# Kernel tuning notes

Hardware: AMD Instinct MI355X
Metric: run time of the kernel (lower is better)

The kernel has to match this reference:

```python
import jax, jax.numpy as jnp
import numpy as np

EPS = 1e-8  # matches torch.nn.functional.cosine_similarity default eps

def setup_inputs() -> dict:
    key = jax.random.key(0)
    k1, k2 = jax.random.split(key)
    x1 = jax.random.normal(k1, (8192, 1024), dtype=jnp.float32)
    x2 = jax.random.normal(k2, (8192, 1024), dtype=jnp.float32)
    return {"x1": x1, "x2": x2}

def reference(x1, x2):
    # cosine_similarity(x1[:,None,:], x2[None,:,:], dim=-1)
    # = (x1 . x2) / (max(||x1||,eps) * max(||x2||,eps))
    # Expressed as normalize-once + GEMM (same math, no [N,M,D] intermediate).
    n1 = jnp.maximum(jnp.linalg.norm(x1, axis=-1, keepdims=True), EPS)  # [N,1]
    n2 = jnp.maximum(jnp.linalg.norm(x2, axis=-1, keepdims=True), EPS)  # [M,1]
    x1n = x1 / n1
    x2n = x2 / n2
    return jnp.einsum('nd,md->nm', x1n, x2n)  # [N,M]
```

## Files before the change

kernel.cpp:

```cpp
#include <hip/hip_runtime.h>
#include <hip/hip_bf16.h>
#include <math.h>


typedef __bf16 bf16x8 __attribute__((ext_vector_type(8)));
typedef float  f32x4  __attribute__((ext_vector_type(4)));

#define LDSP(x) ((__attribute__((address_space(3))) void*)(x))
#define GLBP(x) ((const __attribute__((address_space(1))) void*)(x))

#define BM 256
#define BN 256
#define BK 64
#define EPS_CS 1e-8f


__global__ __launch_bounds__(256) void nrm_bf16_1024_2(const float* __restrict__ in1,
                                                       const float* __restrict__ in2,
                                                       __bf16* __restrict__ out1,
                                                       __bf16* __restrict__ out2,
                                                       int NR) {
    const int r = blockIdx.x;
    const float* in = (r < NR) ? in1 : in2;
    __bf16* out = (r < NR) ? out1 : out2;
    const int row = (r < NR) ? r : r - NR;
    const int t = threadIdx.x;
    const float4 v = reinterpret_cast<const float4*>(in + (size_t)row * 1024)[t];
    float ss = v.x * v.x + v.y * v.y + v.z * v.z + v.w * v.w;
#pragma unroll
    for (int off = 32; off > 0; off >>= 1) ss += __shfl_down(ss, off, 64);
    __shared__ float red[4];
    const int lane = t & 63, wid = t >> 6;
    if (lane == 0) red[wid] = ss;
    __syncthreads();
    const float tot = red[0] + red[1] + red[2] + red[3];
    const float rn = 1.0f / fmaxf(sqrtf(tot), EPS_CS);
    ushort4 pk;
    pk.x = __builtin_bit_cast(unsigned short, (__bf16)(v.x * rn));
    pk.y = __builtin_bit_cast(unsigned short, (__bf16)(v.y * rn));
    pk.z = __builtin_bit_cast(unsigned short, (__bf16)(v.z * rn));
    pk.w = __builtin_bit_cast(unsigned short, (__bf16)(v.w * rn));
    reinterpret_cast<ushort4*>(out + (size_t)row * 1024)[t] = pk;
}


__global__ __launch_bounds__(512, 2) void gemm_nt_bf16_256(const __bf16* __restrict__ A,
                                                           const __bf16* __restrict__ B,
                                                           float* __restrict__ C,
                                                           int NC, int D) {
    __shared__ alignas(16) __bf16 As[2][BM * BK];
    __shared__ alignas(16) __bf16 Bs[2][BN * BK];

    const int t    = threadIdx.x;
    const int lane = t & 63;
    const int wid  = t >> 6;
    const int wm   = wid >> 2;
    const int wn   = wid & 3;
    const int fr   = lane & 15;
    const int fq   = lane >> 4;
    const int xk   = fr & 7;
    const int g0   = fq ^ xk;
    const int g1   = (4 + fq) ^ xk;

    const int nwg = gridDim.x;
    int swz = blockIdx.x;
    if ((nwg & 7) == 0) swz = (swz & 7) * (nwg >> 3) + (swz >> 3);
    const int ntn  = NC / BN;
    const int brow = (swz / ntn) * BM;
    const int bcol = (swz % ntn) * BN;

    const int srow = t >> 3;
    const int sg8  = ((t & 7) ^ (srow & 7)) << 3;
    const __bf16* aSrc = A + (size_t)(brow + srow) * D + sg8;
    const __bf16* bSrc = B + (size_t)(bcol + srow) * D + sg8;
    const int ldsOff = t * 8;

    auto stageA = [&](int buf, int slab, int k) {
        __builtin_amdgcn_global_load_lds(GLBP(aSrc + (size_t)slab * 64 * D + k),
                                         LDSP(&As[buf][slab * 4096 + ldsOff]), 16, 0, 0);
    };
    auto stageB = [&](int buf, int slab, int k) {
        __builtin_amdgcn_global_load_lds(GLBP(bSrc + (size_t)slab * 64 * D + k),
                                         LDSP(&Bs[buf][slab * 4096 + ldsOff]), 16, 0, 0);
    };
    auto ldA = [&](int buf, int mh, int m, int g) {
        const int row = wm * 128 + mh * 64 + m * 16 + fr;
        return *reinterpret_cast<const bf16x8*>(&As[buf][row * 64 + g * 8]);
    };
    auto ldB = [&](int buf, int n, int g) {
        const int row = wn * 64 + n * 16 + fr;
        return *reinterpret_cast<const bf16x8*>(&Bs[buf][row * 64 + g * 8]);
    };

    f32x4 acc[8][4];
#pragma unroll
    for (int i = 0; i < 8; ++i)
#pragma unroll
        for (int n = 0; n < 4; ++n)
            acc[i][n] = (f32x4){0.f, 0.f, 0.f, 0.f};

#pragma unroll
    for (int s = 0; s < 4; ++s) stageB(0, s, 0);
    stageA(0, 0, 0); stageA(0, 2, 0); stageA(0, 1, 0); stageA(0, 3, 0);
    asm volatile("s_waitcnt vmcnt(0)" ::: "memory");
    __builtin_amdgcn_s_barrier();

    const int NT = D / BK;
    int cur = 0;
    for (int kt = 0; kt < NT; ++kt) {
        const int nb = cur ^ 1;
        const int kn = (kt + 1 < NT ? kt + 1 : 0) * BK;
        bf16x8 a[4], b[4];

#pragma unroll
        for (int n = 0; n < 4; ++n) b[n] = ldB(cur, n, g0);
#pragma unroll
        for (int m = 0; m < 4; ++m) a[m] = ldA(cur, 0, m, g0);
        stageB(nb, 0, kn); stageB(nb, 1, kn); stageB(nb, 2, kn); stageB(nb, 3, kn);
        asm volatile("s_waitcnt lgkmcnt(4)" ::: "memory");
        __builtin_amdgcn_s_barrier();
        asm volatile("s_waitcnt lgkmcnt(0)" ::: "memory");
        __builtin_amdgcn_sched_barrier(0);
        __builtin_amdgcn_s_setprio(1);
#pragma unroll
        for (int m = 0; m < 4; ++m)
#pragma unroll
            for (int n = 0; n < 4; ++n)
                acc[m][n] = __builtin_amdgcn_mfma_f32_16x16x32_bf16(a[m], b[n], acc[m][n], 0, 0, 0);
        __builtin_amdgcn_s_setprio(0);
        asm volatile("s_waitcnt vmcnt(4)" ::: "memory");
        __builtin_amdgcn_s_barrier();

#pragma unroll
        for (int m = 0; m < 4; ++m) a[m] = ldA(cur, 1, m, g0);
        stageA(nb, 0, kn); stageA(nb, 2, kn); stageA(nb, 1, kn); stageA(nb, 3, kn);
        __builtin_amdgcn_s_barrier();
        asm volatile("s_waitcnt lgkmcnt(0)" ::: "memory");
        __builtin_amdgcn_sched_barrier(0);
        __builtin_amdgcn_s_setprio(1);
#pragma unroll
        for (int m = 0; m < 4; ++m)
#pragma unroll
            for (int n = 0; n < 4; ++n)
                acc[4 + m][n] = __builtin_amdgcn_mfma_f32_16x16x32_bf16(a[m], b[n], acc[4 + m][n], 0, 0, 0);
        __builtin_amdgcn_s_setprio(0);
        __builtin_amdgcn_s_barrier();

#pragma unroll
        for (int n = 0; n < 4; ++n) b[n] = ldB(cur, n, g1);
#pragma unroll
        for (int m = 0; m < 4; ++m) a[m] = ldA(cur, 0, m, g1);
        asm volatile("s_waitcnt lgkmcnt(4)" ::: "memory");
        __builtin_amdgcn_s_barrier();
        asm volatile("s_waitcnt lgkmcnt(0)" ::: "memory");
        __builtin_amdgcn_sched_barrier(0);
        __builtin_amdgcn_s_setprio(1);
#pragma unroll
        for (int m = 0; m < 4; ++m)
#pragma unroll
            for (int n = 0; n < 4; ++n)
                acc[m][n] = __builtin_amdgcn_mfma_f32_16x16x32_bf16(a[m], b[n], acc[m][n], 0, 0, 0);
        __builtin_amdgcn_s_setprio(0);
        __builtin_amdgcn_s_barrier();

#pragma unroll
        for (int m = 0; m < 4; ++m) a[m] = ldA(cur, 1, m, g1);
        __builtin_amdgcn_s_barrier();
        asm volatile("s_waitcnt lgkmcnt(0)" ::: "memory");
        __builtin_amdgcn_sched_barrier(0);
        __builtin_amdgcn_s_setprio(1);
#pragma unroll
        for (int m = 0; m < 4; ++m)
#pragma unroll
            for (int n = 0; n < 4; ++n)
                acc[4 + m][n] = __builtin_amdgcn_mfma_f32_16x16x32_bf16(a[m], b[n], acc[4 + m][n], 0, 0, 0);
        __builtin_amdgcn_s_setprio(0);
        asm volatile("s_waitcnt vmcnt(2)" ::: "memory");
        __builtin_amdgcn_s_barrier();

        cur = nb;
    }
    asm volatile("s_waitcnt vmcnt(0)" ::: "memory");

    const int crow0 = brow + wm * 128;
    const int ccol0 = bcol + wn * 64;
    const int rr    = fq * 4;
#pragma unroll
    for (int mh = 0; mh < 2; ++mh) {
#pragma unroll
        for (int m = 0; m < 4; ++m) {
#pragma unroll
            for (int r = 0; r < 4; ++r) {
                const size_t rowoff = (size_t)(crow0 + mh * 64 + m * 16 + rr + r) * NC;
#pragma unroll
                for (int n = 0; n < 4; ++n)
                    C[rowoff + ccol0 + n * 16 + fr] = acc[mh * 4 + m][n][r];
            }
        }
    }
}


__global__ __launch_bounds__(256) void rnorm_rows(const float* __restrict__ in,
                                                  float* __restrict__ rn, int D) {
    const int row = blockIdx.x;
    float ss = 0.f;
    for (int c = threadIdx.x; c < D; c += 256) {
        const float v = in[(size_t)row * D + c];
        ss += v * v;
    }
#pragma unroll
    for (int off = 32; off > 0; off >>= 1) ss += __shfl_down(ss, off, 64);
    __shared__ float red[4];
    if ((threadIdx.x & 63) == 0) red[threadIdx.x >> 6] = ss;
    __syncthreads();
    if (threadIdx.x == 0) {
        const float tot = red[0] + red[1] + red[2] + red[3];
        rn[row] = 1.0f / fmaxf(sqrtf(tot), EPS_CS);
    }
}

__global__ __launch_bounds__(256) void gemm_f32_fallback(const float* __restrict__ x1,
                                                         const float* __restrict__ x2,
                                                         const float* __restrict__ rn1,
                                                         const float* __restrict__ rn2,
                                                         float* __restrict__ C,
                                                         int NR, int NC, int D) {
    __shared__ float a[16][17], b[16][17];
    const int tx = threadIdx.x & 15, ty = threadIdx.x >> 4;
    const int row = blockIdx.y * 16 + ty;
    const int colb = blockIdx.x * 16;
    float acc = 0.f;
    for (int k0 = 0; k0 < D; k0 += 16) {
        a[ty][tx] = (row < NR && k0 + tx < D) ? x1[(size_t)row * D + k0 + tx] : 0.f;
        b[ty][tx] = (colb + ty < NC && k0 + tx < D) ? x2[(size_t)(colb + ty) * D + k0 + tx] : 0.f;
        __syncthreads();
#pragma unroll
        for (int k = 0; k < 16; ++k) acc += a[ty][k] * b[tx][k];
        __syncthreads();
    }
    if (row < NR && colb + tx < NC)
        C[(size_t)row * NC + colb + tx] = acc * rn1[row] * rn2[colb + tx];
}


extern "C" void kernel_launch(void* const* d_in, const int* in_sizes, int n_in,
                              void* d_out, int out_size, void* d_ws, size_t ws_size,
                              hipStream_t stream) {
    const float* x1 = (const float*)d_in[0];
    const float* x2 = (const float*)d_in[1];
    float* C = (float*)d_out;

    const int D  = 1024;
    const int NR = in_sizes[0] / D;
    const int NC = in_sizes[1] / D;

    const size_t need = ((size_t)NR + (size_t)NC) * (size_t)D * sizeof(__bf16);
    const bool fast = (in_sizes[0] % D == 0) && (in_sizes[1] % D == 0) &&
                      (NR % BM == 0) && (NC % BN == 0) && (D / BK >= 2) &&
                      (ws_size >= need);

    if (fast) {
        __bf16* An = (__bf16*)d_ws;
        __bf16* Bn = An + (size_t)NR * D;
        nrm_bf16_1024_2<<<NR + NC, 256, 0, stream>>>(x1, x2, An, Bn, NR);
        const int grid = (NR / BM) * (NC / BN);
        gemm_nt_bf16_256<<<grid, 512, 0, stream>>>(An, Bn, C, NC, D);
    } else {
        float* rn1 = (float*)d_ws;
        float* rn2 = rn1 + NR;
        rnorm_rows<<<NR, 256, 0, stream>>>(x1, rn1, D);
        rnorm_rows<<<NC, 256, 0, stream>>>(x2, rn2, D);
        dim3 g((NC + 15) / 16, (NR + 15) / 16);
        gemm_f32_fallback<<<g, 256, 0, stream>>>(x1, x2, rn1, rn2, C, NR, NC, D);
    }
}
```

Measured before the change: 200.3 us.

## Restructure GEMM mainloop into 8-phase quadrant schedule with finer-grained LDS staging

Replaces the 4-phase per-K-tile GEMM loop with an 8-phase loop over two K-tiles. Each phase computes one 128x128 quadrant of the output tile using both K halves at once. The warp-to-output mapping is reorganized so each wave owns interleaved 64x32 sub-blocks across four quadrants. Global-to-LDS copies are split per slab and issued as soon as the buffer region is free, aiming to overlap loads with MFMA work more evenly. The cost is more complex wait counts, a requirement that D be a multiple of 2*BK, and some risk of hazards in the buffer reuse timing.

After: 193.2 us. 3.6% less time.

```diff
diff --git a/kernel.cpp b/kernel.cpp
--- a/kernel.cpp
+++ b/kernel.cpp
@@ -44,7 +44,29 @@
 }
 
 
-__global__ __launch_bounds__(512, 2) void gemm_nt_bf16_256(const __bf16* __restrict__ A,
+#define MFMA_QUAD(MH, NH)                                                          \
+    _Pragma("unroll") for (int mf = 0; mf < 4; ++mf)                               \
+    _Pragma("unroll") for (int nf = 0; nf < 2; ++nf)                               \
+    _Pragma("unroll") for (int ks = 0; ks < 2; ++ks)                               \
+        acc[MH][NH][mf][nf] = __builtin_amdgcn_mfma_f32_16x16x32_bf16(             \
+            aF[mf][ks], bF[nf][ks], acc[MH][NH][mf][nf], 0, 0, 0)
+
+#define OPEN_BAR()                                              \
+    __builtin_amdgcn_s_barrier();                               \
+    asm volatile("s_waitcnt lgkmcnt(0)" ::: "memory");          \
+    __builtin_amdgcn_sched_barrier(0);                          \
+    __builtin_amdgcn_s_setprio(1)
+
+#define CLOSE_BAR()                                             \
+    __builtin_amdgcn_s_setprio(0);                              \
+    __builtin_amdgcn_s_barrier()
+
+#define CLOSE_BAR_VM()                                          \
+    __builtin_amdgcn_s_setprio(0);                              \
+    asm volatile("s_waitcnt vmcnt(6)" ::: "memory");            \
+    __builtin_amdgcn_s_barrier()
+
+__global__ __launch_bounds__(512, 2) void gemm_nt_bf16_8ph(const __bf16* __restrict__ A,
                                                            const __bf16* __restrict__ B,
                                                            float* __restrict__ C,
                                                            int NC, int D) {
@@ -83,121 +105,109 @@
         __builtin_amdgcn_global_load_lds(GLBP(bSrc + (size_t)slab * 64 * D + k),
                                          LDSP(&Bs[buf][slab * 4096 + ldsOff]), 16, 0, 0);
     };
-    auto ldA = [&](int buf, int mh, int m, int g) {
-        const int row = wm * 128 + mh * 64 + m * 16 + fr;
+    auto ldA = [&](int buf, int mh, int mf, int g) {
+        const int row = mh * 128 + wm * 64 + mf * 16 + fr;
         return *reinterpret_cast<const bf16x8*>(&As[buf][row * 64 + g * 8]);
     };
-    auto ldB = [&](int buf, int n, int g) {
-        const int row = wn * 64 + n * 16 + fr;
+    auto ldB = [&](int buf, int nh, int nf, int g) {
+        const int row = nh * 128 + wn * 32 + nf * 16 + fr;
         return *reinterpret_cast<const bf16x8*>(&Bs[buf][row * 64 + g * 8]);
     };
 
-    f32x4 acc[8][4];
-#pragma unroll
-    for (int i = 0; i < 8; ++i)
-#pragma unroll
-        for (int n = 0; n < 4; ++n)
-            acc[i][n] = (f32x4){0.f, 0.f, 0.f, 0.f};
-
-#pragma unroll
-    for (int s = 0; s < 4; ++s) stageB(0, s, 0);
-    stageA(0, 0, 0); stageA(0, 2, 0); stageA(0, 1, 0); stageA(0, 3, 0);
+    f32x4 acc[2][2][4][2];
+#pragma unroll
+    for (int i = 0; i < 2; ++i)
+#pragma unroll
+        for (int j = 0; j < 2; ++j)
+#pragma unroll
+            for (int mf = 0; mf < 4; ++mf)
+#pragma unroll
+                for (int nf = 0; nf < 2; ++nf)
+                    acc[i][j][mf][nf] = (f32x4){0.f, 0.f, 0.f, 0.f};
+
+    bf16x8 aF[4][2], bF[2][2];
+
+    stageA(0, 0, 0); stageA(0, 1, 0);
+    stageB(0, 0, 0); stageB(0, 1, 0);
+    stageB(0, 2, 0); stageB(0, 3, 0);
+    stageA(0, 2, 0); stageA(0, 3, 0);
+    stageA(1, 0, BK); stageA(1, 1, BK);
+    stageB(1, 2, BK); stageB(1, 3, BK);
+    stageA(1, 2, BK); stageA(1, 3, BK);
+    asm volatile("s_waitcnt vmcnt(6)" ::: "memory");
+    __builtin_amdgcn_s_barrier();
+
+    const int NT = D / BK;
+    const int NI = NT >> 1;
+    for (int it = 0; it < NI; ++it) {
+        const int kO  = (2 * it + 1) * BK;
+        const int t2 = 2 * it + 2, t3 = 2 * it + 3;
+        const int kE2 = (t2 < NT) ? t2 * BK : 0;
+        const int kO2 = (t3 < NT) ? t3 * BK : 0;
+
+#pragma unroll
+        for (int mf = 0; mf < 4; ++mf) { aF[mf][0] = ldA(0, 0, mf, g0); aF[mf][1] = ldA(0, 0, mf, g1); }
+#pragma unroll
+        for (int nf = 0; nf < 2; ++nf) { bF[nf][0] = ldB(0, 0, nf, g0); bF[nf][1] = ldB(0, 0, nf, g1); }
+        stageB(1, 0, kO); stageB(1, 1, kO);
+        asm volatile("s_waitcnt lgkmcnt(8)" ::: "memory");
+        OPEN_BAR(); MFMA_QUAD(0, 0); CLOSE_BAR();
+
+#pragma unroll
+        for (int nf = 0; nf < 2; ++nf) { bF[nf][0] = ldB(0, 1, nf, g0); bF[nf][1] = ldB(0, 1, nf, g1); }
+        stageA(0, 0, kE2); stageA(0, 1, kE2);
+        OPEN_BAR(); MFMA_QUAD(0, 1); CLOSE_BAR();
+
+#pragma unroll
+        for (int mf = 0; mf < 4; ++mf) { aF[mf][0] = ldA(0, 1, mf, g0); aF[mf][1] = ldA(0, 1, mf, g1); }
+        stageB(0, 2, kE2); stageB(0, 3, kE2);
+        OPEN_BAR(); MFMA_QUAD(1, 1); CLOSE_BAR();
+
+#pragma unroll
+        for (int nf = 0; nf < 2; ++nf) { bF[nf][0] = ldB(0, 0, nf, g0); bF[nf][1] = ldB(0, 0, nf, g1); }
+        stageA(0, 2, kE2); stageA(0, 3, kE2);
+        OPEN_BAR(); MFMA_QUAD(1, 0); CLOSE_BAR_VM();
+
+#pragma unroll
+        for (int mf = 0; mf < 4; ++mf) { aF[mf][0] = ldA(1, 0, mf, g0); aF[mf][1] = ldA(1, 0, mf, g1); }
+#pragma unroll
+        for (int nf = 0; nf < 2; ++nf) { bF[nf][0] = ldB(1, 0, nf, g0); bF[nf][1] = ldB(1, 0, nf, g1); }
+        stageB(0, 0, kE2); stageB(0, 1, kE2);
+        asm volatile("s_waitcnt lgkmcnt(8)" ::: "memory");
+        OPEN_BAR(); MFMA_QUAD(0, 0); CLOSE_BAR();
+
+#pragma unroll
+        for (int nf = 0; nf < 2; ++nf) { bF[nf][0] = ldB(1, 1, nf, g0); bF[nf][1] = ldB(1, 1, nf, g1); }
+        stageA(1, 0, kO2); stageA(1, 1, kO2);
+        OPEN_BAR(); MFMA_QUAD(0, 1); CLOSE_BAR();
+
+#pragma unroll
+        for (int mf = 0; mf < 4; ++mf) { aF[mf][0] = ldA(1, 1, mf, g0); aF[mf][1] = ldA(1, 1, mf, g1); }
+        stageB(1, 2, kO2); stageB(1, 3, kO2);
+        OPEN_BAR(); MFMA_QUAD(1, 1); CLOSE_BAR();
+
+#pragma unroll
+        for (int nf = 0; nf < 2; ++nf) { bF[nf][0] = ldB(1, 0, nf, g0); bF[nf][1] = ldB(1, 0, nf, g1); }
+        stageA(1, 2, kO2); stageA(1, 3, kO2);
+        OPEN_BAR(); MFMA_QUAD(1, 0); CLOSE_BAR_VM();
+    }
     asm volatile("s_waitcnt vmcnt(0)" ::: "memory");
-    __builtin_amdgcn_s_barrier();
-
-    const int NT = D / BK;
-    int cur = 0;
-    for (int kt = 0; kt < NT; ++kt) {
-        const int nb = cur ^ 1;
-        const int kn = (kt + 1 < NT ? kt + 1 : 0) * BK;
-        bf16x8 a[4], b[4];
-
-#pragma unroll
-        for (int n = 0; n < 4; ++n) b[n] = ldB(cur, n, g0);
-#pragma unroll
-        for (int m = 0; m < 4; ++m) a[m] = ldA(cur, 0, m, g0);
-        stageB(nb, 0, kn); stageB(nb, 1, kn); stageB(nb, 2, kn); stageB(nb, 3, kn);
-        asm volatile("s_waitcnt lgkmcnt(4)" ::: "memory");
-        __builtin_amdgcn_s_barrier();
-        asm volatile("s_waitcnt lgkmcnt(0)" ::: "memory");
-        __builtin_amdgcn_sched_barrier(0);
-        __builtin_amdgcn_s_setprio(1);
-#pragma unroll
-        for (int m = 0; m < 4; ++m)
-#pragma unroll
-            for (int n = 0; n < 4; ++n)
-                acc[m][n] = __builtin_amdgcn_mfma_f32_16x16x32_bf16(a[m], b[n], acc[m][n], 0, 0, 0);
-        __builtin_amdgcn_s_setprio(0);
-        asm volatile("s_waitcnt vmcnt(4)" ::: "memory");
-        __builtin_amdgcn_s_barrier();
-
-#pragma unroll
-        for (int m = 0; m < 4; ++m) a[m] = ldA(cur, 1, m, g0);
-        stageA(nb, 0, kn); stageA(nb, 2, kn); stageA(nb, 1, kn); stageA(nb, 3, kn);
-        __builtin_amdgcn_s_barrier();
-        asm volatile("s_waitcnt lgkmcnt(0)" ::: "memory");
-        __builtin_amdgcn_sched_barrier(0);
-        __builtin_amdgcn_s_setprio(1);
-#pragma unroll
-        for (int m = 0; m < 4; ++m)
-#pragma unroll
-            for (int n = 0; n < 4; ++n)
-                acc[4 + m][n] = __builtin_amdgcn_mfma_f32_16x16x32_bf16(a[m], b[n], acc[4 + m][n], 0, 0, 0);
-        __builtin_amdgcn_s_setprio(0);
-        __builtin_amdgcn_s_barrier();
-
-#pragma unroll
-        for (int n = 0; n < 4; ++n) b[n] = ldB(cur, n, g1);
-#pragma unroll
-        for (int m = 0; m < 4; ++m) a[m] = ldA(cur, 0, m, g1);
-        asm volatile("s_waitcnt lgkmcnt(4)" ::: "memory");
-        __builtin_amdgcn_s_barrier();
-        asm volatile("s_waitcnt lgkmcnt(0)" ::: "memory");
-        __builtin_amdgcn_sched_barrier(0);
-        __builtin_amdgcn_s_setprio(1);
-#pragma unroll
-        for (int m = 0; m < 4; ++m)
-#pragma unroll
-            for (int n = 0; n < 4; ++n)
-                acc[m][n] = __builtin_amdgcn_mfma_f32_16x16x32_bf16(a[m], b[n], acc[m][n], 0, 0, 0);
-        __builtin_amdgcn_s_setprio(0);
-        __builtin_amdgcn_s_barrier();
-
-#pragma unroll
-        for (int m = 0; m < 4; ++m) a[m] = ldA(cur, 1, m, g1);
-        __builtin_amdgcn_s_barrier();
-        asm volatile("s_waitcnt lgkmcnt(0)" ::: "memory");
-        __builtin_amdgcn_sched_barrier(0);
-        __builtin_amdgcn_s_setprio(1);
-#pragma unroll
-        for (int m = 0; m < 4; ++m)
-#pragma unroll
-            for (int n = 0; n < 4; ++n)
-                acc[4 + m][n] = __builtin_amdgcn_mfma_f32_16x16x32_bf16(a[m], b[n], acc[4 + m][n], 0, 0, 0);
-        __builtin_amdgcn_s_setprio(0);
-        asm volatile("s_waitcnt vmcnt(2)" ::: "memory");
-        __builtin_amdgcn_s_barrier();
-
-        cur = nb;
-    }
-    asm volatile("s_waitcnt vmcnt(0)" ::: "memory");
-
-    const int crow0 = brow + wm * 128;
-    const int ccol0 = bcol + wn * 64;
-    const int rr    = fq * 4;
-#pragma unroll
-    for (int mh = 0; mh < 2; ++mh) {
-#pragma unroll
-        for (int m = 0; m < 4; ++m) {
-#pragma unroll
-            for (int r = 0; r < 4; ++r) {
-                const size_t rowoff = (size_t)(crow0 + mh * 64 + m * 16 + rr + r) * NC;
-#pragma unroll
-                for (int n = 0; n < 4; ++n)
-                    C[rowoff + ccol0 + n * 16 + fr] = acc[mh * 4 + m][n][r];
-            }
-        }
-    }
+
+#pragma unroll
+    for (int mh = 0; mh < 2; ++mh)
+#pragma unroll
+        for (int nh = 0; nh < 2; ++nh)
+#pragma unroll
+            for (int mf = 0; mf < 4; ++mf)
+#pragma unroll
+                for (int r = 0; r < 4; ++r) {
+                    const size_t rowoff =
+                        (size_t)(brow + mh * 128 + wm * 64 + mf * 16 + fq * 4 + r) * NC;
+#pragma unroll
+                    for (int nf = 0; nf < 2; ++nf)
+                        C[rowoff + bcol + nh * 128 + wn * 32 + nf * 16 + fr] =
+                            acc[mh][nh][mf][nf][r];
+                }
 }
 
 
@@ -257,15 +267,15 @@
 
     const size_t need = ((size_t)NR + (size_t)NC) * (size_t)D * sizeof(__bf16);
     const bool fast = (in_sizes[0] % D == 0) && (in_sizes[1] % D == 0) &&
-                      (NR % BM == 0) && (NC % BN == 0) && (D / BK >= 2) &&
-                      (ws_size >= need);
+                      (NR % BM == 0) && (NC % BN == 0) &&
+                      (D % (2 * BK) == 0) && (ws_size >= need);
 
     if (fast) {
         __bf16* An = (__bf16*)d_ws;
         __bf16* Bn = An + (size_t)NR * D;
         nrm_bf16_1024_2<<<NR + NC, 256, 0, stream>>>(x1, x2, An, Bn, NR);
         const int grid = (NR / BM) * (NC / BN);
-        gemm_nt_bf16_256<<<grid, 512, 0, stream>>>(An, Bn, C, NC, D);
+        gemm_nt_bf16_8ph<<<grid, 512, 0, stream>>>(An, Bn, C, NC, D);
     } else {
         float* rn1 = (float*)d_ws;
         float* rn2 = rn1 + NR;
```
